# Performance work log

Measured on AMD Instinct MI355X. Metric: run time of the kernel, lower is better.

The kernel has to match this reference:

```python
import jax, jax.numpy as jnp
import numpy as np

N, E, D, L = 100000, 640000, 128, 3
EPS = 1e-5


def setup_inputs() -> dict:
    key = jax.random.key(0)
    ks = jax.random.split(key, 12)
    s = 1.0 / np.sqrt(D)
    return {
        "x": jax.random.normal(ks[0], (N, D), dtype=jnp.float32),
        "edge_index": jax.random.randint(ks[1], (2, E), 0, N, dtype=jnp.int64),
        "conv_w": jax.random.normal(ks[2], (L, D, D), dtype=jnp.float32) * s,
        "conv_b": jnp.zeros((L, D), dtype=jnp.float32),
        "gn_weight": jnp.ones((L, D), dtype=jnp.float32),
        "gn_bias": jnp.zeros((L, D), dtype=jnp.float32),
        "gn_mean_scale": jnp.ones((L, D), dtype=jnp.float32),
        "proj_w": jax.random.normal(ks[3], (D, D), dtype=jnp.float32) * s,
        "mlp_w": jax.random.normal(ks[4], (D, D), dtype=jnp.float32) * s,
        "mlp_b": jnp.zeros((D,), dtype=jnp.float32),
        "head_w": jax.random.normal(ks[5], (D, 1), dtype=jnp.float32) * s,
        "head_b": jnp.zeros((1,), dtype=jnp.float32),
    }


def _graph_norm(h, w, b, ms):
    # PyG GraphNorm over a single graph: subtract learnable-scaled mean, divide by std.
    mean = jnp.mean(h, axis=0)
    out = h - ms * mean
    var = jnp.mean(out * out, axis=0)
    return out / jnp.sqrt(var + EPS) * w + b


def reference(x, edge_index, conv_w, conv_b, gn_weight, gn_bias, gn_mean_scale,
              proj_w, mlp_w, mlp_b, head_w, head_b):
    n = x.shape[0]
    loop = jnp.arange(n, dtype=edge_index.dtype)
    row = jnp.concatenate([edge_index[0], loop])  # source
    col = jnp.concatenate([edge_index[1], loop])  # destination
    deg = jax.ops.segment_sum(jnp.ones_like(col, dtype=x.dtype), col, num_segments=n)
    dinv = jnp.where(deg > 0, jax.lax.rsqrt(deg), 0.0)
    norm = dinv[row] * dinv[col]  # [E+N]

    def gcn_conv(h, W, b):
        hw = h @ W                          # [N, D]
        msg = hw[row] * norm[:, None]       # gather + scale, [E+N, D]
        return jax.ops.segment_sum(msg, col, num_segments=n) + b

    h1 = x
    for i in range(L):
        residual = h1 @ proj_w if i == 0 else x  # shared_source skip
        h = gcn_conv(x, conv_w[i], conv_b[i])
        h = _graph_norm(h, gn_weight[i], gn_bias[i], gn_mean_scale[i])
        x = jax.nn.relu(h) + residual

    x = jax.nn.relu(x @ mlp_w + mlp_b)      # shared MLP (one layer for sizes [D, D])
    return x @ head_w + head_b              # task head -> [N, 1]
```

## Files before the change

kernel.cpp:

```cpp
#include <hip/hip_runtime.h>

#define FD 128

typedef __attribute__((ext_vector_type(8))) short bf16x8;
typedef __attribute__((ext_vector_type(4))) float f32x4;

__device__ __forceinline__ unsigned short f2bf(float f) {
  unsigned int u = __float_as_uint(f);
  unsigned int r = (u + 0x7fffu + ((u >> 16) & 1u)) >> 16;
  return (unsigned short)r;
}
__device__ __forceinline__ float bf_lo(unsigned int u) { return __uint_as_float(u << 16); }
__device__ __forceinline__ float bf_hi(unsigned int u) { return __uint_as_float(u & 0xffff0000u); }
__device__ __forceinline__ unsigned int pack_bf2(float a, float b) {
  return (unsigned int)f2bf(a) | ((unsigned int)f2bf(b) << 16);
}
__device__ __forceinline__ float bf2f_us(unsigned short s) { return __uint_as_float(((unsigned int)s) << 16); }

__global__ __launch_bounds__(256) void init_kernel(int* __restrict__ deg, int* __restrict__ fill,
    float* __restrict__ stats, int n) {
  int i = blockIdx.x * 256 + threadIdx.x;
  if (i < n) { deg[i] = 1; fill[i] = 0; }
  if (i < 768) stats[i] = 0.f;
}

__global__ __launch_bounds__(256) void edge_count_kernel(const int* __restrict__ ei, int e, int* __restrict__ deg) {
  int i = blockIdx.x * 256 + threadIdx.x;
  if (i < e) atomicAdd(&deg[ei[e + i]], 1);
}

__global__ __launch_bounds__(128) void scan1_kernel(const int* __restrict__ deg, int n,
    int* __restrict__ tmp, int* __restrict__ partials, float* __restrict__ dinv) {
  __shared__ int s[128];
  int b = blockIdx.x, t = threadIdx.x;
  int i = b * 128 + t;
  int d = (i < n) ? deg[i] : 1;
  if (i < n) dinv[i] = rsqrtf((float)d);
  s[t] = (i < n) ? (d - 1) : 0;
  __syncthreads();
  for (int off = 1; off < 128; off <<= 1) {
    int u = (t >= off) ? s[t - off] : 0;
    __syncthreads();
    s[t] += u;
    __syncthreads();
  }
  if (i < n) tmp[i] = s[t];
  if (t == 127) partials[b] = s[127];
}

__global__ __launch_bounds__(1024) void scan2_kernel(int* __restrict__ partials, int nb) {
  __shared__ int s[1024];
  int t = threadIdx.x;
  s[t] = (t < nb) ? partials[t] : 0;
  __syncthreads();
  for (int off = 1; off < 1024; off <<= 1) {
    int u = (t >= off) ? s[t - off] : 0;
    __syncthreads();
    s[t] += u;
    __syncthreads();
  }
  if (t < nb) partials[t] = (t == 0) ? 0 : s[t - 1];
}

__global__ __launch_bounds__(128) void scan3_kernel(const int* __restrict__ tmp, const int* __restrict__ partials, int* __restrict__ indptr, int n) {
  int i = blockIdx.x * 128 + threadIdx.x;
  if (i < n) indptr[i + 1] = tmp[i] + partials[blockIdx.x];
  if (i == 0) indptr[0] = 0;
}

__global__ __launch_bounds__(256) void fill_kernel(const int* __restrict__ ei, int e,
    const int* __restrict__ indptr, int* __restrict__ fill, const float* __restrict__ dinv,
    int* __restrict__ csr_src, float* __restrict__ csr_norm) {
  int i = blockIdx.x * 256 + threadIdx.x;
  if (i < e) {
    int r = ei[i];
    int c = ei[e + i];
    int pos = indptr[c] + atomicAdd(&fill[c], 1);
    csr_src[pos] = r;
    csr_norm[pos] = dinv[r] * dinv[c];
  }
}

__global__ __launch_bounds__(256) void prep_w(const float* __restrict__ conv_w, const float* __restrict__ proj_w,
    const float* __restrict__ mlp_w, unsigned short* __restrict__ Wtb) {
  int idx = blockIdx.x * 256 + threadIdx.x;
  int m = idx >> 14;
  int o = idx & 16383;
  int col = o >> 7, k = o & 127;
  const float* src = (m < 3) ? (conv_w + m * 16384) : ((m == 3) ? proj_w : mlp_w);
  Wtb[idx] = f2bf(src[k * FD + col]);
}

__global__ __launch_bounds__(256) void convert_x0(const float* __restrict__ x, unsigned int* __restrict__ xb, int total2) {
  int i = blockIdx.x * blockDim.x + threadIdx.x;
  int stride = gridDim.x * blockDim.x;
  for (; i < total2; i += stride) {
    float2 v = ((const float2*)x)[i];
    xb[i] = pack_bf2(v.x, v.y);
  }
}

template<int EPI, bool FUSEA>
__global__ __launch_bounds__(256) void mfma_gemm(const unsigned short* __restrict__ Ab,
    const unsigned short* __restrict__ Wtb, void* __restrict__ Cout, int n,
    const unsigned short* __restrict__ aggb, const float* __restrict__ sv, const float* __restrict__ tv,
    const float* __restrict__ bias, const float* __restrict__ hw, const float* __restrict__ hb,
    const float* __restrict__ svA, const float* __restrict__ tvA,
    const unsigned short* __restrict__ residA, unsigned short* __restrict__ xout)
{
  __shared__ uint4 bsh[2048];
  const int tid = threadIdx.x;
  const int l = tid & 63;
  const int w = tid >> 6;
  const int row0 = blockIdx.x * 64 + w * 16;

  #pragma unroll
  for (int it = 0; it < 8; ++it) {
    int s = it * 256 + tid;
    int nf = s >> 8, kf = (s >> 6) & 3, sl = s & 63;
    int col = nf * 16 + (sl & 15);
    bsh[s] = *(const uint4*)(Wtb + col * FD + kf * 32 + (sl >> 4) * 8);
  }

  const int arow = row0 + (l & 15);
  bf16x8 a[4];
  if (arow < n) {
    if (FUSEA) {
      const uint4* agp = (const uint4*)(Ab + (size_t)arow * FD + (l >> 4) * 8);
      const uint4* rsp = (const uint4*)(residA + (size_t)arow * FD + (l >> 4) * 8);
      uint4* xop = xout ? (uint4*)(xout + (size_t)arow * FD + (l >> 4) * 8) : nullptr;
      #pragma unroll
      for (int kf = 0; kf < 4; ++kf) {
        uint4 ag = agp[kf * 4];
        uint4 rs = rsp[kf * 4];
        int cb4 = kf * 8 + (l >> 4) * 2;
        float4 s0 = ((const float4*)svA)[cb4];
        float4 s1 = ((const float4*)svA)[cb4 + 1];
        float4 t0 = ((const float4*)tvA)[cb4];
        float4 t1 = ((const float4*)tvA)[cb4 + 1];
        uint4 pk;
        pk.x = pack_bf2(fmaxf(fmaf(bf_lo(ag.x), s0.x, t0.x), 0.f) + bf_lo(rs.x),
                        fmaxf(fmaf(bf_hi(ag.x), s0.y, t0.y), 0.f) + bf_hi(rs.x));
        pk.y = pack_bf2(fmaxf(fmaf(bf_lo(ag.y), s0.z, t0.z), 0.f) + bf_lo(rs.y),
                        fmaxf(fmaf(bf_hi(ag.y), s0.w, t0.w), 0.f) + bf_hi(rs.y));
        pk.z = pack_bf2(fmaxf(fmaf(bf_lo(ag.z), s1.x, t1.x), 0.f) + bf_lo(rs.z),
                        fmaxf(fmaf(bf_hi(ag.z), s1.y, t1.y), 0.f) + bf_hi(rs.z));
        pk.w = pack_bf2(fmaxf(fmaf(bf_lo(ag.w), s1.z, t1.z), 0.f) + bf_lo(rs.w),
                        fmaxf(fmaf(bf_hi(ag.w), s1.w, t1.w), 0.f) + bf_hi(rs.w));
        a[kf] = *(bf16x8*)&pk;
        if (xop) xop[kf * 4] = pk;
      }
    } else {
      const uint4* ap = (const uint4*)(Ab + (size_t)arow * FD + (l >> 4) * 8);
      #pragma unroll
      for (int kf = 0; kf < 4; ++kf) { uint4 t = ap[kf * 4]; a[kf] = *(bf16x8*)&t; }
    }
  } else {
    #pragma unroll
    for (int kf = 0; kf < 4; ++kf) a[kf] = (bf16x8)(short)0;
  }

  __syncthreads();

  f32x4 acc[8];
  #pragma unroll
  for (int nf = 0; nf < 8; ++nf) acc[nf] = (f32x4)(0.0f);

  #pragma unroll
  for (int nf = 0; nf < 8; ++nf) {
    #pragma unroll
    for (int kf = 0; kf < 4; ++kf) {
      uint4 braw = bsh[(nf * 4 + kf) * 64 + l];
      acc[nf] = __builtin_amdgcn_mfma_f32_16x16x32_bf16(a[kf], *(bf16x8*)&braw, acc[nf], 0, 0, 0);
    }
  }

  if (EPI == 2) {
    float hsum[4] = {0.f, 0.f, 0.f, 0.f};
    #pragma unroll
    for (int nf = 0; nf < 8; ++nf) {
      int col = nf * 16 + (l & 15);
      float bm = bias[col];
      float hwc = hw[col];
      #pragma unroll
      for (int i = 0; i < 4; ++i)
        hsum[i] += fmaxf(acc[nf][i] + bm, 0.f) * hwc;
    }
    #pragma unroll
    for (int i = 0; i < 4; ++i) {
      #pragma unroll
      for (int off = 1; off < 16; off <<= 1) hsum[i] += __shfl_xor(hsum[i], off);
    }
    if ((l & 15) == 0) {
      float hb0 = hb[0];
      #pragma unroll
      for (int i = 0; i < 4; ++i) {
        int r = row0 + (l >> 4) * 4 + i;
        if (r < n) ((float*)Cout)[r] = hsum[i] + hb0;
      }
    }
  } else {
    unsigned short* outp = (unsigned short*)Cout;
    #pragma unroll
    for (int nf = 0; nf < 8; ++nf) {
      int col = nf * 16 + (l & 15);
      float s = (EPI == 1) ? sv[col] : 0.f;
      float t = (EPI == 1) ? tv[col] : 0.f;
      #pragma unroll
      for (int i = 0; i < 4; ++i) {
        int r = row0 + (l >> 4) * 4 + i;
        if (r < n) {
          float v = acc[nf][i];
          if (EPI == 1) {
            float ag = bf2f_us(aggb[(size_t)r * FD + col]);
            v += fmaxf(fmaf(ag, s, t), 0.f);
          }
          outp[(size_t)r * FD + col] = f2bf(v);
        }
      }
    }
  }
}

__device__ __forceinline__ void acc8(float* a, uint4 u, float wn) {
  a[0] = fmaf(wn, bf_lo(u.x), a[0]); a[1] = fmaf(wn, bf_hi(u.x), a[1]);
  a[2] = fmaf(wn, bf_lo(u.y), a[2]); a[3] = fmaf(wn, bf_hi(u.y), a[3]);
  a[4] = fmaf(wn, bf_lo(u.z), a[4]); a[5] = fmaf(wn, bf_hi(u.z), a[5]);
  a[6] = fmaf(wn, bf_lo(u.w), a[6]); a[7] = fmaf(wn, bf_hi(u.w), a[7]);
}

__global__ __launch_bounds__(256) void agg_bf16(const uint4* __restrict__ hw4, uint4* __restrict__ agg4,
    const int* __restrict__ indptr, const int* __restrict__ csr_src, const float* __restrict__ csr_norm,
    const float* __restrict__ dinv, const float* __restrict__ bias,
    float* __restrict__ colsum, float* __restrict__ colsum2, int n)
{
  __shared__ float sredS[4][16][9];
  __shared__ float sredQ[4][16][9];
  const int wv = threadIdx.x >> 6;
  const int lane = threadIdx.x & 63;
  const int q = lane >> 4;
  const int l16 = lane & 15;
  const int gs = blockIdx.x * 16 + wv * 4 + q;
  const int ns = gridDim.x * 16;
  const float4 b0 = ((const float4*)bias)[l16 * 2];
  const float4 b1 = ((const float4*)bias)[l16 * 2 + 1];
  float st[8], sq[8];
  #pragma unroll
  for (int j = 0; j < 8; ++j) { st[j] = 0.f; sq[j] = 0.f; }

  int c = gs;
  float di = 0.f; int e0 = 0, e1 = 0;
  uint4 su = make_uint4(0, 0, 0, 0);
  if (c < n) {
    di = dinv[c];
    e0 = indptr[c]; e1 = indptr[c + 1];
    su = hw4[(size_t)c * 16 + l16];
  }
  while (c < n) {
    const int cn = c + ns;
    float di_n = 0.f; int e0_n = 0, e1_n = 0;
    uint4 su_n = make_uint4(0, 0, 0, 0);
    if (cn < n) {
      di_n = dinv[cn];
      e0_n = indptr[cn]; e1_n = indptr[cn + 1];
      su_n = hw4[(size_t)cn * 16 + l16];
    }

    float self = di * di;
    float a[8];
    a[0] = fmaf(self, bf_lo(su.x), b0.x); a[1] = fmaf(self, bf_hi(su.x), b0.y);
    a[2] = fmaf(self, bf_lo(su.y), b0.z); a[3] = fmaf(self, bf_hi(su.y), b0.w);
    a[4] = fmaf(self, bf_lo(su.z), b1.x); a[5] = fmaf(self, bf_hi(su.z), b1.y);
    a[6] = fmaf(self, bf_lo(su.w), b1.z); a[7] = fmaf(self, bf_hi(su.w), b1.w);
    int e = e0;
    for (; e + 4 <= e1; e += 4) {
      int s0 = csr_src[e], s1 = csr_src[e + 1], s2 = csr_src[e + 2], s3 = csr_src[e + 3];
      float w0 = csr_norm[e], w1 = csr_norm[e + 1], w2 = csr_norm[e + 2], w3 = csr_norm[e + 3];
      uint4 u0 = hw4[(size_t)s0 * 16 + l16];
      uint4 u1 = hw4[(size_t)s1 * 16 + l16];
      uint4 u2 = hw4[(size_t)s2 * 16 + l16];
      uint4 u3 = hw4[(size_t)s3 * 16 + l16];
      acc8(a, u0, w0); acc8(a, u1, w1); acc8(a, u2, w2); acc8(a, u3, w3);
    }
    if (e + 2 <= e1) {
      int s0 = csr_src[e], s1 = csr_src[e + 1];
      float w0 = csr_norm[e], w1 = csr_norm[e + 1];
      uint4 u0 = hw4[(size_t)s0 * 16 + l16];
      uint4 u1 = hw4[(size_t)s1 * 16 + l16];
      acc8(a, u0, w0); acc8(a, u1, w1);
      e += 2;
    }
    if (e < e1) {
      int s0 = csr_src[e];
      float w0 = csr_norm[e];
      uint4 u0 = hw4[(size_t)s0 * 16 + l16];
      acc8(a, u0, w0);
    }
    uint4 o;
    o.x = pack_bf2(a[0], a[1]); o.y = pack_bf2(a[2], a[3]);
    o.z = pack_bf2(a[4], a[5]); o.w = pack_bf2(a[6], a[7]);
    agg4[(size_t)c * 16 + l16] = o;
    #pragma unroll
    for (int j = 0; j < 8; ++j) { st[j] += a[j]; sq[j] += a[j] * a[j]; }

    c = cn; di = di_n; e0 = e0_n; e1 = e1_n; su = su_n;
  }

  #pragma unroll
  for (int j = 0; j < 8; ++j) {
    st[j] += __shfl_xor(st[j], 16); st[j] += __shfl_xor(st[j], 32);
    sq[j] += __shfl_xor(sq[j], 16); sq[j] += __shfl_xor(sq[j], 32);
  }
  if (q == 0) {
    #pragma unroll
    for (int j = 0; j < 8; ++j) { sredS[wv][l16][j] = st[j]; sredQ[wv][l16][j] = sq[j]; }
  }
  __syncthreads();
  int t = threadIdx.x;
  int which = t >> 7, cc = t & 127;
  int rl = cc >> 3, rk = cc & 7;
  float v = 0.f;
  #pragma unroll
  for (int w2 = 0; w2 < 4; ++w2)
    v += which ? sredQ[w2][rl][rk] : sredS[w2][rl][rk];
  atomicAdd(which ? &colsum2[cc] : &colsum[cc], v);
}

__global__ void finalize_stats(const float* __restrict__ colsum, const float* __restrict__ colsum2,
    const float* __restrict__ gnw, const float* __restrict__ gnb, const float* __restrict__ ms,
    float* __restrict__ sv, float* __restrict__ tv, float inv_n)
{
  int d = threadIdx.x;
  if (d < FD) {
    float mean = colsum[d] * inv_n;
    float m2 = colsum2[d] * inv_n;
    float m = ms[d];
    float var = m2 - 2.f * m * mean * mean + m * m * mean * mean;
    float s = gnw[d] * rsqrtf(var + 1e-5f);
    sv[d] = s;
    tv[d] = gnb[d] - m * mean * s;
  }
}

extern "C" void kernel_launch(void* const* d_in, const int* in_sizes, int n_in,
                              void* d_out, int out_size, void* d_ws, size_t ws_size,
                              hipStream_t stream) {
  const float* x0      = (const float*)d_in[0];
  const int* ei        = (const int*)d_in[1];
  const float* conv_w  = (const float*)d_in[2];
  const float* conv_b  = (const float*)d_in[3];
  const float* gn_w    = (const float*)d_in[4];
  const float* gn_b    = (const float*)d_in[5];
  const float* gn_ms   = (const float*)d_in[6];
  const float* proj_w  = (const float*)d_in[7];
  const float* mlp_w   = (const float*)d_in[8];
  const float* mlp_b   = (const float*)d_in[9];
  const float* head_w  = (const float*)d_in[10];
  const float* head_b  = (const float*)d_in[11];
  float* out = (float*)d_out;

  const int n = in_sizes[0] / FD;
  const int e = in_sizes[1] / 2;
  const size_t ND = (size_t)n * FD;

  unsigned short* xb0  = (unsigned short*)d_ws;
  unsigned short* xb1  = xb0 + ND;
  unsigned short* hwb  = xb1 + ND;
  unsigned short* aggb = hwb + ND;
  unsigned short* Wtb  = aggb + ND;
  float* csr_norm = (float*)(Wtb + 5 * 16384);
  float* dinv     = csr_norm + e;
  float* stats    = dinv + n;
  float* sv       = stats + 768;
  float* tv       = sv + FD;
  int* deg     = (int*)(tv + FD);
  int* fill    = deg + n;
  int* indptr  = fill + n;
  int* tmp     = indptr + (n + 1);
  int* partials= tmp + n;
  int* csr_src = partials + 1024;

  const int nb256_n = (n + 255) / 256;
  const int nb256_e = (e + 255) / 256;
  const int nb128_n = (n + 127) / 128;

  init_kernel<<<nb256_n, 256, 0, stream>>>(deg, fill, stats, n);
  edge_count_kernel<<<nb256_e, 256, 0, stream>>>(ei, e, deg);
  scan1_kernel<<<nb128_n, 128, 0, stream>>>(deg, n, tmp, partials, dinv);
  scan2_kernel<<<1, 1024, 0, stream>>>(partials, nb128_n);
  scan3_kernel<<<nb128_n, 128, 0, stream>>>(tmp, partials, indptr, n);
  fill_kernel<<<nb256_e, 256, 0, stream>>>(ei, e, indptr, fill, dinv, csr_src, csr_norm);

  prep_w<<<320, 256, 0, stream>>>(conv_w, proj_w, mlp_w, Wtb);
  convert_x0<<<2048, 256, 0, stream>>>(x0, (unsigned int*)xb0, (int)(ND / 2));

  const int gemm_grid = (n + 63) / 64;
  const float inv_n = 1.f / (float)n;
  const unsigned short* Wt_conv0 = Wtb;
  const unsigned short* Wt_conv1 = Wtb + 16384;
  const unsigned short* Wt_conv2 = Wtb + 2 * 16384;
  const unsigned short* Wt_proj  = Wtb + 3 * 16384;
  const unsigned short* Wt_mlp   = Wtb + 4 * 16384;

  mfma_gemm<0, false><<<gemm_grid, 256, 0, stream>>>(xb0, Wt_conv0, hwb, n,
      nullptr, nullptr, nullptr, nullptr, nullptr, nullptr, nullptr, nullptr, nullptr, nullptr);
  agg_bf16<<<2048, 256, 0, stream>>>((const uint4*)hwb, (uint4*)aggb, indptr, csr_src, csr_norm, dinv,
                                     conv_b + 0 * FD, stats + 0 * FD, stats + 384 + 0 * FD, n);
  finalize_stats<<<1, 128, 0, stream>>>(stats + 0 * FD, stats + 384 + 0 * FD,
      gn_w + 0 * FD, gn_b + 0 * FD, gn_ms + 0 * FD, sv, tv, inv_n);
  mfma_gemm<1, false><<<gemm_grid, 256, 0, stream>>>(xb0, Wt_proj, xb1, n,
      aggb, sv, tv, nullptr, nullptr, nullptr, nullptr, nullptr, nullptr, nullptr);

  mfma_gemm<0, false><<<gemm_grid, 256, 0, stream>>>(xb1, Wt_conv1, hwb, n,
      nullptr, nullptr, nullptr, nullptr, nullptr, nullptr, nullptr, nullptr, nullptr, nullptr);
  agg_bf16<<<2048, 256, 0, stream>>>((const uint4*)hwb, (uint4*)aggb, indptr, csr_src, csr_norm, dinv,
                                     conv_b + 1 * FD, stats + 1 * FD, stats + 384 + 1 * FD, n);
  finalize_stats<<<1, 128, 0, stream>>>(stats + 1 * FD, stats + 384 + 1 * FD,
      gn_w + 1 * FD, gn_b + 1 * FD, gn_ms + 1 * FD, sv, tv, inv_n);

  mfma_gemm<0, true><<<gemm_grid, 256, 0, stream>>>(aggb, Wt_conv2, hwb, n,
      nullptr, nullptr, nullptr, nullptr, nullptr, nullptr, sv, tv, xb1, xb0);
  agg_bf16<<<2048, 256, 0, stream>>>((const uint4*)hwb, (uint4*)aggb, indptr, csr_src, csr_norm, dinv,
                                     conv_b + 2 * FD, stats + 2 * FD, stats + 384 + 2 * FD, n);
  finalize_stats<<<1, 128, 0, stream>>>(stats + 2 * FD, stats + 384 + 2 * FD,
      gn_w + 2 * FD, gn_b + 2 * FD, gn_ms + 2 * FD, sv, tv, inv_n);

  mfma_gemm<2, true><<<gemm_grid, 256, 0, stream>>>(aggb, Wt_mlp, out, n,
      nullptr, nullptr, nullptr, mlp_b, head_w, head_b, sv, tv, xb0, nullptr);
}
```

Baseline: 410.4 us.

## Fuse x0 conversion and dual conv0/proj GEMM into one kernel

Drops the separate fp32-to-bf16 conversion pass over x0. A new dual GEMM reads x0 in fp32, converts it in registers, and computes both the conv0 product and the projection product from the same A fragments, storing the projection residual separately. The layer-0 epilogue that added relu(norm(agg)) into the proj output is moved into the A-load prologue of the next conv GEMM. That removes one full GEMM read pass and a bf16 intermediate write, but the dual kernel reads fp32 input at twice the bytes and keeps an extra ND buffer.

```diff
diff --git a/kernel.cpp b/kernel.cpp
--- a/kernel.cpp
+++ b/kernel.cpp
@@ -15,7 +15,6 @@
 __device__ __forceinline__ unsigned int pack_bf2(float a, float b) {
   return (unsigned int)f2bf(a) | ((unsigned int)f2bf(b) << 16);
 }
-__device__ __forceinline__ float bf2f_us(unsigned short s) { return __uint_as_float(((unsigned int)s) << 16); }
 
 __global__ __launch_bounds__(256) void init_kernel(int* __restrict__ deg, int* __restrict__ fill,
     float* __restrict__ stats, int n) {
@@ -91,19 +90,99 @@
   Wtb[idx] = f2bf(src[k * FD + col]);
 }
 
-__global__ __launch_bounds__(256) void convert_x0(const float* __restrict__ x, unsigned int* __restrict__ xb, int total2) {
-  int i = blockIdx.x * blockDim.x + threadIdx.x;
-  int stride = gridDim.x * blockDim.x;
-  for (; i < total2; i += stride) {
-    float2 v = ((const float2*)x)[i];
-    xb[i] = pack_bf2(v.x, v.y);
-  }
-}
-
-template<int EPI, bool FUSEA>
+__global__ __launch_bounds__(256) void gemm_dual(const float* __restrict__ x0,
+    const unsigned short* __restrict__ W0t, const unsigned short* __restrict__ Pt,
+    unsigned short* __restrict__ hw0, unsigned short* __restrict__ xp, int n)
+{
+  __shared__ uint4 bsh[2048];
+  const int tid = threadIdx.x;
+  const int l = tid & 63;
+  const int w = tid >> 6;
+  const int row0 = blockIdx.x * 64 + w * 16;
+
+  #pragma unroll
+  for (int it = 0; it < 8; ++it) {
+    int s = it * 256 + tid;
+    int nf = s >> 8, kf = (s >> 6) & 3, sl = s & 63;
+    int col = nf * 16 + (sl & 15);
+    bsh[s] = *(const uint4*)(W0t + col * FD + kf * 32 + (sl >> 4) * 8);
+  }
+
+  const int arow = row0 + (l & 15);
+  bf16x8 a[4];
+  if (arow < n) {
+    const float4* ap = (const float4*)(x0 + (size_t)arow * FD + (l >> 4) * 8);
+    #pragma unroll
+    for (int kf = 0; kf < 4; ++kf) {
+      float4 f0 = ap[kf * 8];
+      float4 f1 = ap[kf * 8 + 1];
+      uint4 pk;
+      pk.x = pack_bf2(f0.x, f0.y); pk.y = pack_bf2(f0.z, f0.w);
+      pk.z = pack_bf2(f1.x, f1.y); pk.w = pack_bf2(f1.z, f1.w);
+      a[kf] = *(bf16x8*)&pk;
+    }
+  } else {
+    #pragma unroll
+    for (int kf = 0; kf < 4; ++kf) a[kf] = (bf16x8)(short)0;
+  }
+
+  __syncthreads();
+
+  f32x4 acc[8];
+  #pragma unroll
+  for (int nf = 0; nf < 8; ++nf) acc[nf] = (f32x4)(0.0f);
+  #pragma unroll
+  for (int nf = 0; nf < 8; ++nf)
+    #pragma unroll
+    for (int kf = 0; kf < 4; ++kf) {
+      uint4 braw = bsh[(nf * 4 + kf) * 64 + l];
+      acc[nf] = __builtin_amdgcn_mfma_f32_16x16x32_bf16(a[kf], *(bf16x8*)&braw, acc[nf], 0, 0, 0);
+    }
+
+  __syncthreads();
+
+  #pragma unroll
+  for (int it = 0; it < 8; ++it) {
+    int s = it * 256 + tid;
+    int nf = s >> 8, kf = (s >> 6) & 3, sl = s & 63;
+    int col = nf * 16 + (sl & 15);
+    bsh[s] = *(const uint4*)(Pt + col * FD + kf * 32 + (sl >> 4) * 8);
+  }
+  #pragma unroll
+  for (int nf = 0; nf < 8; ++nf) {
+    int col = nf * 16 + (l & 15);
+    #pragma unroll
+    for (int i = 0; i < 4; ++i) {
+      int r = row0 + (l >> 4) * 4 + i;
+      if (r < n) hw0[(size_t)r * FD + col] = f2bf(acc[nf][i]);
+    }
+  }
+
+  __syncthreads();
+
+  #pragma unroll
+  for (int nf = 0; nf < 8; ++nf) acc[nf] = (f32x4)(0.0f);
+  #pragma unroll
+  for (int nf = 0; nf < 8; ++nf)
+    #pragma unroll
+    for (int kf = 0; kf < 4; ++kf) {
+      uint4 braw = bsh[(nf * 4 + kf) * 64 + l];
+      acc[nf] = __builtin_amdgcn_mfma_f32_16x16x32_bf16(a[kf], *(bf16x8*)&braw, acc[nf], 0, 0, 0);
+    }
+  #pragma unroll
+  for (int nf = 0; nf < 8; ++nf) {
+    int col = nf * 16 + (l & 15);
+    #pragma unroll
+    for (int i = 0; i < 4; ++i) {
+      int r = row0 + (l >> 4) * 4 + i;
+      if (r < n) xp[(size_t)r * FD + col] = f2bf(acc[nf][i]);
+    }
+  }
+}
+
+template<int EPI>
 __global__ __launch_bounds__(256) void mfma_gemm(const unsigned short* __restrict__ Ab,
     const unsigned short* __restrict__ Wtb, void* __restrict__ Cout, int n,
-    const unsigned short* __restrict__ aggb, const float* __restrict__ sv, const float* __restrict__ tv,
     const float* __restrict__ bias, const float* __restrict__ hw, const float* __restrict__ hb,
     const float* __restrict__ svA, const float* __restrict__ tvA,
     const unsigned short* __restrict__ residA, unsigned short* __restrict__ xout)
@@ -125,35 +204,29 @@
   const int arow = row0 + (l & 15);
   bf16x8 a[4];
   if (arow < n) {
-    if (FUSEA) {
-      const uint4* agp = (const uint4*)(Ab + (size_t)arow * FD + (l >> 4) * 8);
-      const uint4* rsp = (const uint4*)(residA + (size_t)arow * FD + (l >> 4) * 8);
-      uint4* xop = xout ? (uint4*)(xout + (size_t)arow * FD + (l >> 4) * 8) : nullptr;
-      #pragma unroll
-      for (int kf = 0; kf < 4; ++kf) {
-        uint4 ag = agp[kf * 4];
-        uint4 rs = rsp[kf * 4];
-        int cb4 = kf * 8 + (l >> 4) * 2;
-        float4 s0 = ((const float4*)svA)[cb4];
-        float4 s1 = ((const float4*)svA)[cb4 + 1];
-        float4 t0 = ((const float4*)tvA)[cb4];
-        float4 t1 = ((const float4*)tvA)[cb4 + 1];
-        uint4 pk;
-        pk.x = pack_bf2(fmaxf(fmaf(bf_lo(ag.x), s0.x, t0.x), 0.f) + bf_lo(rs.x),
-                        fmaxf(fmaf(bf_hi(ag.x), s0.y, t0.y), 0.f) + bf_hi(rs.x));
-        pk.y = pack_bf2(fmaxf(fmaf(bf_lo(ag.y), s0.z, t0.z), 0.f) + bf_lo(rs.y),
-                        fmaxf(fmaf(bf_hi(ag.y), s0.w, t0.w), 0.f) + bf_hi(rs.y));
-        pk.z = pack_bf2(fmaxf(fmaf(bf_lo(ag.z), s1.x, t1.x), 0.f) + bf_lo(rs.z),
-                        fmaxf(fmaf(bf_hi(ag.z), s1.y, t1.y), 0.f) + bf_hi(rs.z));
-        pk.w = pack_bf2(fmaxf(fmaf(bf_lo(ag.w), s1.z, t1.z), 0.f) + bf_lo(rs.w),
-                        fmaxf(fmaf(bf_hi(ag.w), s1.w, t1.w), 0.f) + bf_hi(rs.w));
-        a[kf] = *(bf16x8*)&pk;
-        if (xop) xop[kf * 4] = pk;
-      }
-    } else {
-      const uint4* ap = (const uint4*)(Ab + (size_t)arow * FD + (l >> 4) * 8);
-      #pragma unroll
-      for (int kf = 0; kf < 4; ++kf) { uint4 t = ap[kf * 4]; a[kf] = *(bf16x8*)&t; }
+    const uint4* agp = (const uint4*)(Ab + (size_t)arow * FD + (l >> 4) * 8);
+    const uint4* rsp = (const uint4*)(residA + (size_t)arow * FD + (l >> 4) * 8);
+    uint4* xop = xout ? (uint4*)(xout + (size_t)arow * FD + (l >> 4) * 8) : nullptr;
+    #pragma unroll
+    for (int kf = 0; kf < 4; ++kf) {
+      uint4 ag = agp[kf * 4];
+      uint4 rs = rsp[kf * 4];
+      int cb4 = kf * 8 + (l >> 4) * 2;
+      float4 s0 = ((const float4*)svA)[cb4];
+      float4 s1 = ((const float4*)svA)[cb4 + 1];
+      float4 t0 = ((const float4*)tvA)[cb4];
+      float4 t1 = ((const float4*)tvA)[cb4 + 1];
+      uint4 pk;
+      pk.x = pack_bf2(fmaxf(fmaf(bf_lo(ag.x), s0.x, t0.x), 0.f) + bf_lo(rs.x),
+                      fmaxf(fmaf(bf_hi(ag.x), s0.y, t0.y), 0.f) + bf_hi(rs.x));
+      pk.y = pack_bf2(fmaxf(fmaf(bf_lo(ag.y), s0.z, t0.z), 0.f) + bf_lo(rs.y),
+                      fmaxf(fmaf(bf_hi(ag.y), s0.w, t0.w), 0.f) + bf_hi(rs.y));
+      pk.z = pack_bf2(fmaxf(fmaf(bf_lo(ag.z), s1.x, t1.x), 0.f) + bf_lo(rs.z),
+                      fmaxf(fmaf(bf_hi(ag.z), s1.y, t1.y), 0.f) + bf_hi(rs.z));
+      pk.w = pack_bf2(fmaxf(fmaf(bf_lo(ag.w), s1.z, t1.z), 0.f) + bf_lo(rs.w),
+                      fmaxf(fmaf(bf_hi(ag.w), s1.w, t1.w), 0.f) + bf_hi(rs.w));
+      a[kf] = *(bf16x8*)&pk;
+      if (xop) xop[kf * 4] = pk;
     }
   } else {
     #pragma unroll
@@ -165,15 +238,13 @@
   f32x4 acc[8];
   #pragma unroll
   for (int nf = 0; nf < 8; ++nf) acc[nf] = (f32x4)(0.0f);
-
-  #pragma unroll
-  for (int nf = 0; nf < 8; ++nf) {
+  #pragma unroll
+  for (int nf = 0; nf < 8; ++nf)
     #pragma unroll
     for (int kf = 0; kf < 4; ++kf) {
       uint4 braw = bsh[(nf * 4 + kf) * 64 + l];
       acc[nf] = __builtin_amdgcn_mfma_f32_16x16x32_bf16(a[kf], *(bf16x8*)&braw, acc[nf], 0, 0, 0);
     }
-  }
 
   if (EPI == 2) {
     float hsum[4] = {0.f, 0.f, 0.f, 0.f};
@@ -204,19 +275,10 @@
     #pragma unroll
     for (int nf = 0; nf < 8; ++nf) {
       int col = nf * 16 + (l & 15);
-      float s = (EPI == 1) ? sv[col] : 0.f;
-      float t = (EPI == 1) ? tv[col] : 0.f;
       #pragma unroll
       for (int i = 0; i < 4; ++i) {
         int r = row0 + (l >> 4) * 4 + i;
-        if (r < n) {
-          float v = acc[nf][i];
-          if (EPI == 1) {
-            float ag = bf2f_us(aggb[(size_t)r * FD + col]);
-            v += fmaxf(fmaf(ag, s, t), 0.f);
-          }
-          outp[(size_t)r * FD + col] = f2bf(v);
-        }
+        if (r < n) outp[(size_t)r * FD + col] = f2bf(acc[nf][i]);
       }
     }
   }
@@ -363,11 +425,11 @@
   const int e = in_sizes[1] / 2;
   const size_t ND = (size_t)n * FD;
 
-  unsigned short* xb0  = (unsigned short*)d_ws;
-  unsigned short* xb1  = xb0 + ND;
-  unsigned short* hwb  = xb1 + ND;
+  unsigned short* hwb  = (unsigned short*)d_ws;
   unsigned short* aggb = hwb + ND;
-  unsigned short* Wtb  = aggb + ND;
+  unsigned short* xpb  = aggb + ND;
+  unsigned short* xrb  = xpb + ND;
+  unsigned short* Wtb  = xrb + ND;
   float* csr_norm = (float*)(Wtb + 5 * 16384);
   float* dinv     = csr_norm + e;
   float* stats    = dinv + n;
@@ -392,7 +454,6 @@
   fill_kernel<<<nb256_e, 256, 0, stream>>>(ei, e, indptr, fill, dinv, csr_src, csr_norm);
 
   prep_w<<<320, 256, 0, stream>>>(conv_w, proj_w, mlp_w, Wtb);
-  convert_x0<<<2048, 256, 0, stream>>>(x0, (unsigned int*)xb0, (int)(ND / 2));
 
   const int gemm_grid = (n + 63) / 64;
   const float inv_n = 1.f / (float)n;
@@ -402,29 +463,26 @@
   const unsigned short* Wt_proj  = Wtb + 3 * 16384;
   const unsigned short* Wt_mlp   = Wtb + 4 * 16384;
 
-  mfma_gemm<0, false><<<gemm_grid, 256, 0, stream>>>(xb0, Wt_conv0, hwb, n,
-      nullptr, nullptr, nullptr, nullptr, nullptr, nullptr, nullptr, nullptr, nullptr, nullptr);
+  gemm_dual<<<gemm_grid, 256, 0, stream>>>(x0, Wt_conv0, Wt_proj, hwb, xpb, n);
   agg_bf16<<<2048, 256, 0, stream>>>((const uint4*)hwb, (uint4*)aggb, indptr, csr_src, csr_norm, dinv,
                                      conv_b + 0 * FD, stats + 0 * FD, stats + 384 + 0 * FD, n);
   finalize_stats<<<1, 128, 0, stream>>>(stats + 0 * FD, stats + 384 + 0 * FD,
       gn_w + 0 * FD, gn_b + 0 * FD, gn_ms + 0 * FD, sv, tv, inv_n);
-  mfma_gemm<1, false><<<gemm_grid, 256, 0, stream>>>(xb0, Wt_proj, xb1, n,
-      aggb, sv, tv, nullptr, nullptr, nullptr, nullptr, nullptr, nullptr, nullptr);
-
-  mfma_gemm<0, false><<<gemm_grid, 256, 0, stream>>>(xb1, Wt_conv1, hwb, n,
-      nullptr, nullptr, nullptr, nullptr, nullptr, nullptr, nullptr, nullptr, nullptr, nullptr);
+
+  mfma_gemm<0><<<gemm_grid, 256, 0, stream>>>(aggb, Wt_conv1, hwb, n,
+      nullptr, nullptr, nullptr, sv, tv, xpb, xrb);
   agg_bf16<<<2048, 256, 0, stream>>>((const uint4*)hwb, (uint4*)aggb, indptr, csr_src, csr_norm, dinv,
                                      conv_b + 1 * FD, stats + 1 * FD, stats + 384 + 1 * FD, n);
   finalize_stats<<<1, 128, 0, stream>>>(stats + 1 * FD, stats + 384 + 1 * FD,
       gn_w + 1 * FD, gn_b + 1 * FD, gn_ms + 1 * FD, sv, tv, inv_n);
 
-  mfma_gemm<0, true><<<gemm_grid, 256, 0, stream>>>(aggb, Wt_conv2, hwb, n,
-      nullptr, nullptr, nullptr, nullptr, nullptr, nullptr, sv, tv, xb1, xb0);
+  mfma_gemm<0><<<gemm_grid, 256, 0, stream>>>(aggb, Wt_conv2, hwb, n,
+      nullptr, nullptr, nullptr, sv, tv, xrb, xpb);
   agg_bf16<<<2048, 256, 0, stream>>>((const uint4*)hwb, (uint4*)aggb, indptr, csr_src, csr_norm, dinv,
                                      conv_b + 2 * FD, stats + 2 * FD, stats + 384 + 2 * FD, n);
   finalize_stats<<<1, 128, 0, stream>>>(stats + 2 * FD, stats + 384 + 2 * FD,
       gn_w + 2 * FD, gn_b + 2 * FD, gn_ms + 2 * FD, sv, tv, inv_n);
 
-  mfma_gemm<2, true><<<gemm_grid, 256, 0, stream>>>(aggb, Wt_mlp, out, n,
-      nullptr, nullptr, nullptr, mlp_b, head_w, head_b, sv, tv, xb0, nullptr);
-}
+  mfma_gemm<2><<<gemm_grid, 256, 0, stream>>>(aggb, Wt_mlp, out, n,
+      mlp_b, head_w, head_b, sv, tv, xpb, nullptr);
+}
```

Result: faster. 401.0 us (-2.3%).
